# Kernel tuning notes

Measured on AMD Instinct MI355X. Metric: run time of the kernel, lower is better.

Reference implementation:

```python
import jax, jax.numpy as jnp
import numpy as np
from jax import lax

B = 512
THRESHOLD = 0.5
CFG = [64, 64, 'M', 128, 128, 'M', 256, 256, 256, 'M', 512, 512, 512, 'M', 512, 512, 512, 'M']  # VGG16


def _conv_relu(x, w, b):
    # x: [B,C,H,W], w: [O,I,3,3] (torch OIHW layout), pad=1 stride=1
    y = lax.conv_general_dilated(x, w, (1, 1), 'SAME',
                                 dimension_numbers=('NCHW', 'OIHW', 'NCHW'))
    return jax.nn.relu(y + b[None, :, None, None])


def _maxpool2(x):
    return lax.reduce_window(x, -jnp.inf, lax.max, (1, 1, 2, 2), (1, 1, 2, 2), 'VALID')


def _features(x, ws, bs):
    i = 0
    for c in CFG:
        if c == 'M':
            x = _maxpool2(x)
        else:
            x = _conv_relu(x, ws[i], bs[i])
            i += 1
    return x  # [B,512,1,1]


def _gcn(distance):
    # Faithful translation, including the source bug: 'onetensor' is zeros_like,
    # so mask==0 everywhere and A_hat collapses to the identity.
    n = distance.shape[0]
    zero = jnp.zeros_like(distance)
    one = jnp.zeros_like(distance)  # bug in original: torch.zeros_like for onetensor
    adj = jnp.where(distance > THRESHOLD, distance, zero)
    mask = jnp.where(distance > THRESHOLD, one, zero)
    idx = lax.top_k(adj, 10)[1]                                   # [n,10]
    top10 = jnp.zeros_like(adj).at[jnp.arange(n)[:, None], idx].set(1.0)
    top10 = top10 * mask
    a_hat = top10 + jnp.eye(n, dtype=distance.dtype)
    d_inv = jnp.diag(1.0 / jnp.sum(a_hat, axis=1))
    return lax.stop_gradient(a_hat @ d_inv)                        # [n,n]


def _forward(x, target, conv_ws, conv_bs, lin1_w, lin1_b, lin2_w, lin2_b, cls_w, cls_b):
    feat = _features(x, conv_ws, conv_bs).reshape(x.shape[0], -1)  # [B,512]
    h = jax.nn.relu(feat @ lin1_w + lin1_b)                        # [B,256]
    low = h @ lin2_w + lin2_b                                      # [B,128]
    graph_pre = jax.nn.sigmoid(low @ low.T)                        # [B,B]
    graph_gt = (target[:, None] == target[None, :]).astype(jnp.float32)
    mat = _gcn(graph_pre)                                          # [B,B], detached
    out = (mat @ feat) @ cls_w + cls_b                             # [B,10]
    return out, graph_pre, graph_gt


def setup_inputs() -> dict:
    key = jax.random.key(0)
    ks = iter(jax.random.split(key, 64))
    inp = {}
    inp['x'] = jax.random.normal(next(ks), (B, 3, 32, 32), dtype=jnp.float32)
    inp['target'] = jax.random.randint(next(ks), (B,), 0, 10)
    in_c, i = 3, 0
    for c in CFG:
        if c == 'M':
            continue
        scale = 1.0 / np.sqrt(in_c * 9.0)
        inp['conv%d_w' % i] = jax.random.normal(next(ks), (c, in_c, 3, 3), dtype=jnp.float32) * scale
        inp['conv%d_b' % i] = jnp.zeros((c,), dtype=jnp.float32)
        in_c, i = c, i + 1
    inp['lin1_w'] = jax.random.normal(next(ks), (512, 256), dtype=jnp.float32) * (1.0 / np.sqrt(512.0))
    inp['lin1_b'] = jnp.zeros((256,), dtype=jnp.float32)
    inp['lin2_w'] = jax.random.normal(next(ks), (256, 128), dtype=jnp.float32) * (1.0 / np.sqrt(256.0))
    inp['lin2_b'] = jnp.zeros((128,), dtype=jnp.float32)
    inp['cls_w'] = jax.random.normal(next(ks), (512, 10), dtype=jnp.float32) * (1.0 / np.sqrt(512.0))
    inp['cls_b'] = jnp.zeros((10,), dtype=jnp.float32)
    return inp


def reference(x, target,
              conv0_w, conv0_b, conv1_w, conv1_b, conv2_w, conv2_b, conv3_w, conv3_b,
              conv4_w, conv4_b, conv5_w, conv5_b, conv6_w, conv6_b, conv7_w, conv7_b,
              conv8_w, conv8_b, conv9_w, conv9_b, conv10_w, conv10_b, conv11_w, conv11_b,
              conv12_w, conv12_b,
              lin1_w, lin1_b, lin2_w, lin2_b, cls_w, cls_b):
    ws = [conv0_w, conv1_w, conv2_w, conv3_w, conv4_w, conv5_w, conv6_w,
          conv7_w, conv8_w, conv9_w, conv10_w, conv11_w, conv12_w]
    bs = [conv0_b, conv1_b, conv2_b, conv3_b, conv4_b, conv5_b, conv6_b,
          conv7_b, conv8_b, conv9_b, conv10_b, conv11_b, conv12_b]
    return _forward(x, target, ws, bs, lin1_w, lin1_b, lin2_w, lin2_b, cls_w, cls_b)
```

## Files before the change

kernel.cpp:

```cpp
#include <hip/hip_runtime.h>

typedef unsigned short u16;
typedef __bf16 bf16x8 __attribute__((ext_vector_type(8)));
typedef float floatx4 __attribute__((ext_vector_type(4)));

__device__ inline u16 f2bf(float f) {
    return __builtin_bit_cast(u16, (__bf16)f);
}
__device__ inline float bf2f(u16 h) {
    return __uint_as_float(((unsigned int)h) << 16);
}

__device__ __forceinline__ void async_copy16(u16* lds, const u16* g) {
    __builtin_amdgcn_global_load_lds(
        (const __attribute__((address_space(1))) unsigned int*)(uintptr_t)g,
        (__attribute__((address_space(3))) unsigned int*)(unsigned int)(uintptr_t)lds,
        16, 0, 0);
}

__global__ void zero_halo(u16* __restrict__ buf, int Hp, int C, int total8)
{
    int i = blockIdx.x * 256 + threadIdx.x;
    if (i >= total8) return;
    int c8 = i % (C / 8);
    int p  = i / (C / 8);
    int ring = 4 * Hp - 4;
    int h = p % ring;
    int b = p / ring;
    int y, x;
    if (h < Hp)              { y = 0;              x = h; }
    else if (h < 2 * Hp)     { y = Hp - 1;         x = h - Hp; }
    else if (h < 3 * Hp - 2) { y = h - 2 * Hp + 1; x = 0; }
    else                     { y = h - 3 * Hp + 3; x = Hp - 1; }
    uint4 z = make_uint4(0u, 0u, 0u, 0u);
    *(uint4*)(buf + ((size_t)((b * Hp + y) * Hp + x) * C) + c8 * 8) = z;
}

__global__ __launch_bounds__(256) void conv0_mfma(
    const float* __restrict__ x, const float* __restrict__ w,
    const float* __restrict__ bias, u16* __restrict__ out)
{
    __shared__ __align__(16) float xsf[3 * 10 * 36];
    __shared__ int tab[32];
    const int t  = threadIdx.x;
    const int b  = blockIdx.x >> 2;
    const int y0 = (blockIdx.x & 3) * 8;

    for (int i = t; i < 3 * 10 * 36; i += 256) {
        int ci  = i / 360;
        int rem = i % 360;
        int r   = rem / 36;
        int c   = rem % 36;
        int gy  = y0 - 1 + r;
        int gx  = c - 1;
        float v = 0.f;
        if ((unsigned)gy < 32u && (unsigned)gx < 32u)
            v = x[((b * 3 + ci) * 32 + gy) * 32 + gx];
        xsf[i] = v;
    }
    if (t < 32) {
        int k = t, off = 0;
        if (k < 27) {
            int ci = k / 9;
            int r9 = k - ci * 9;
            int rr = r9 / 3;
            int cc = r9 - rr * 3;
            off = (ci * 10 + rr) * 36 + cc;
        }
        tab[t] = off;
    }

    const int lane = t & 63;
    const int wv   = t >> 6;
    const int quad = lane >> 4;
    const int l16  = lane & 15;
    const int q8   = quad * 8;

    bf16x8 bf[4];
    #pragma unroll
    for (int nt = 0; nt < 4; nt++) {
        int col = nt * 16 + l16;
        u16 hh[8];
        #pragma unroll
        for (int j = 0; j < 8; j++) {
            int k = q8 + j;
            float wv_ = (k < 27) ? w[col * 27 + k] : 0.f;
            hh[j] = f2bf(wv_);
        }
        #pragma unroll
        for (int j = 0; j < 8; j++) ((u16*)&bf[nt])[j] = hh[j];
    }
    float bzv[4];
    #pragma unroll
    for (int nt = 0; nt < 4; nt++) bzv[nt] = bias[nt * 16 + l16];

    __syncthreads();

    int tb_[8];
    #pragma unroll
    for (int j = 0; j < 8; j++) tb_[j] = tab[q8 + j];

    bf16x8 af[4];
    #pragma unroll
    for (int mt = 0; mt < 4; mt++) {
        int dm   = wv * 64 + mt * 16 + l16;
        int yloc = dm >> 5;
        int xx   = dm & 31;
        int bix  = yloc * 36 + xx;
        u16 hh[8];
        #pragma unroll
        for (int j = 0; j < 8; j++) hh[j] = f2bf(xsf[bix + tb_[j]]);
        if (quad == 3) {
            #pragma unroll
            for (int j = 3; j < 8; j++) hh[j] = 0;
        }
        #pragma unroll
        for (int j = 0; j < 8; j++) ((u16*)&af[mt])[j] = hh[j];
    }

    floatx4 acc[4][4];
    #pragma unroll
    for (int i = 0; i < 4; i++)
        #pragma unroll
        for (int j = 0; j < 4; j++)
            acc[i][j] = (floatx4){0.f, 0.f, 0.f, 0.f};

    #pragma unroll
    for (int mt = 0; mt < 4; mt++)
        #pragma unroll
        for (int nt = 0; nt < 4; nt++)
            acc[mt][nt] = __builtin_amdgcn_mfma_f32_16x16x32_bf16(
                af[mt], bf[nt], acc[mt][nt], 0, 0, 0);

    #pragma unroll
    for (int mt = 0; mt < 4; mt++) {
        #pragma unroll
        for (int r = 0; r < 4; r++) {
            int p  = wv * 64 + mt * 16 + quad * 4 + r;
            int y  = y0 + (p >> 5);
            int xx = p & 31;
            u16* op = out + (size_t)((b * 34 + y + 1) * 34 + xx + 1) * 64 + l16;
            #pragma unroll
            for (int nt = 0; nt < 4; nt++)
                op[nt * 16] = f2bf(fmaxf(acc[mt][nt][r] + bzv[nt], 0.f));
        }
    }
}

struct RepackArgs {
    const float* src[14];
    u16* dst[14];
    int p1[14];
    int p2[14];
    int startBlk[15];
    int nseg;
};

__global__ __launch_bounds__(256) void repack_all(RepackArgs a)
{
    __shared__ __align__(16) u16 lds[9216];
    int blk = blockIdx.x;
    int s = 0;
    #pragma unroll 1
    while (s + 1 < a.nseg && blk >= a.startBlk[s + 1]) s++;
    const int cb = blk - a.startBlk[s];
    const int t  = threadIdx.x;

    if (a.p2[s] == 0) {
        const int Cin = a.p1[s];
        const int logCin = __builtin_ctz(Cin);
        const float* src = a.src[s] + (size_t)cb * 9216;
        u16* dst = a.dst[s] + (size_t)cb * 9216;
        #pragma unroll
        for (int it = 0; it < 9; it++) {
            int j4 = it * 256 + t;
            float4 v = *(const float4*)(src + j4 * 4);
            ushort4 h;
            h.x = f2bf(v.x); h.y = f2bf(v.y); h.z = f2bf(v.z); h.w = f2bf(v.w);
            *(ushort4*)(lds + j4 * 4) = h;
        }
        __syncthreads();
        #pragma unroll
        for (int it = 0; it < 9; it++) {
            int o4   = (it * 256 + t) * 4;
            int ci   = o4 & (Cin - 1);
            int rest = o4 >> logCin;
            int co   = rest / 9;
            int sh   = rest - co * 9;
            int sb   = (co << logCin) * 9 + ci * 9 + sh;
            ushort4 h;
            h.x = lds[sb]; h.y = lds[sb + 9]; h.z = lds[sb + 18]; h.w = lds[sb + 27];
            *(ushort4*)(dst + o4) = h;
        }
    } else {
        const int K = a.p1[s], N = a.p2[s];
        const int ntx = N >> 6;
        const int k0 = (cb / ntx) * 64, n0 = (cb % ntx) * 64;
        const float* src = a.src[s];
        u16* dst = a.dst[s];
        const int r = t >> 4, c4 = (t & 15) * 4;
        #pragma unroll
        for (int rr = 0; rr < 64; rr += 16) {
            float4 v = *(const float4*)(src + (size_t)(k0 + r + rr) * N + n0 + c4);
            u16* p = lds + (r + rr) * 72 + c4;
            p[0] = f2bf(v.x); p[1] = f2bf(v.y); p[2] = f2bf(v.z); p[3] = f2bf(v.w);
        }
        __syncthreads();
        #pragma unroll
        for (int it = 0; it < 2; it++) {
            int ov = it * 256 + t;
            int n  = ov >> 3;
            int kq = (ov & 7) * 8;
            __align__(16) u16 h[8];
            #pragma unroll
            for (int j = 0; j < 8; j++) h[j] = lds[(kq + j) * 72 + n];
            *(uint4*)(dst + (size_t)(n0 + n) * K + k0 + kq) = *(uint4*)h;
        }
    }
}

struct FragArgs {
    const u16* src[3];
    u16* dst[3];
    int cin[3];
    int logwn[3];
    int total[3];
    int startBlk[4];
};

__global__ __launch_bounds__(256) void repack_frag(FragArgs a)
{
    int blk = blockIdx.x;
    int s = 0;
    #pragma unroll 1
    while (s + 1 < 3 && blk >= a.startBlk[s + 1]) s++;
    int i = (blk - a.startBlk[s]) * 256 + threadIdx.x;
    if (i >= a.total[s]) return;
    const int LOGWN = a.logwn[s];
    int l16  = i & 15;
    int quad = (i >> 4) & 3;
    int nt   = (i >> 6) & 3;
    int wn   = (i >> 8) & ((1 << LOGWN) - 1);
    int kk2  = (i >> (8 + LOGWN)) & 1;
    int it   = i >> (9 + LOGWN);
    int col  = wn * 64 + nt * 16 + l16;
    int k    = it * 64 + (kk2 * 4 + quad) * 8;
    uint4 v = *(const uint4*)(a.src[s] + (size_t)col * 9 * a.cin[s] + k);
    *(uint4*)(a.dst[s] + (size_t)i * 8) = v;
}

template <int BM, int BN>
__global__ __launch_bounds__(256) void conv_gemm(
    const u16* __restrict__ in, const u16* __restrict__ wt,
    const float* __restrict__ bias, u16* __restrict__ out,
    float* __restrict__ partial, size_t pstride,
    int H, int Cin, int Cout, int logHW, int logW, int splitN,
    int outPad, int poolMode)
{
    constexpr int BK = 64;
    constexpr int WC = (BM == 256) ? BN : (BN / 2);
    constexpr int NT = WC / 16;
    constexpr int NB_A = BM / 32;
    constexpr int NB_B = BN / 32;
    constexpr int ASZ = BM * BK;
    constexpr int BSZ = BN * BK;
    __shared__ u16 As[2 * ASZ];
    __shared__ u16 Bs[2 * BSZ];

    const int Nblocks = Cout / BN;
    const int per = gridDim.x >> 3;
    const int bid = (blockIdx.x & 7) * per + (blockIdx.x >> 3);
    const int sp   = bid % splitN;
    const int tile = bid / splitN;
    const int m0 = (tile / Nblocks) * BM;
    const int n0 = (tile % Nblocks) * BN;

    const int t    = threadIdx.x;
    const int lane = t & 63;
    const int wave = t >> 6;
    const int quad = lane >> 4;
    const int l16  = lane & 15;
    const int wm   = (BM == 256) ? wave : (wave >> 1);
    const int wn   = (BM == 256) ? 0 : (wave & 1);
    const int W    = H;
    const int Wp   = H + 2;
    const int HW   = 1 << logHW;
    const int col8 = t & 7;
    const int r0   = t >> 3;
    const int scol = col8 ^ (r0 & 7);

    const int CinB = Cin * 2;

    int vA[NB_A];
    #pragma unroll
    for (int j = 0; j < NB_A; j++) {
        int m  = m0 + r0 + 32 * j;
        int b  = m >> logHW;
        int rm = m & (HW - 1);
        int y  = rm >> logW;
        int xx = rm & (W - 1);
        vA[j] = ((b * Wp + y + 1) * Wp + xx + 1) * CinB + scol * 16;
    }
    int vB[NB_B];
    #pragma unroll
    for (int j = 0; j < NB_B; j++)
        vB[j] = (n0 + r0 + 32 * j) * 9 * CinB + scol * 16;

    const int logKB = (Cin == 64) ? 0 : (Cin == 128) ? 1 : (Cin == 256) ? 2 : 3;
    const int KB  = 1 << logKB;
    const int T   = 9 * KB;
    const int len = T / splitN;
    const int it0 = sp * len;

    int s0 = it0 >> logKB;
    int c3 = s0 - (s0 / 3) * 3;
    int ta = ((s0 / 3 - 1) * Wp + (c3 - 1)) * CinB;
    int kb = (it0 & (KB - 1)) * 128;
    int tb = it0 * 128;

    const char* const inB = (const char*)in;
    const char* const wtB = (const char*)wt;

    floatx4 acc[4][NT];
    #pragma unroll
    for (int i = 0; i < 4; i++)
        #pragma unroll
        for (int j = 0; j < NT; j++)
            acc[i][j] = (floatx4){0.f, 0.f, 0.f, 0.f};

    const int sw = (l16 & 7) * 8;

    auto stage = [&](int ua, int tbv, int buf) {
        u16* la = As + buf * ASZ + t * 8;
        u16* lb = Bs + buf * BSZ + t * 8;
        #pragma unroll
        for (int j = 0; j < NB_A; j++)
            async_copy16(la + j * 2048, (const u16*)(inB + (ua + vA[j])));
        #pragma unroll
        for (int j = 0; j < NB_B; j++)
            async_copy16(lb + j * 2048, (const u16*)(wtB + (tbv + vB[j])));
    };
    auto advance = [&]() {
        tb += 128;
        kb += 128;
        if (kb == CinB) {
            kb = 0;
            ta += (c3 == 2) ? (Wp - 2) * CinB : CinB;
            c3 = (c3 == 2) ? 0 : c3 + 1;
        }
    };

    stage(ta + kb, tb, 0);
    advance();
    __syncthreads();

    int cur = 0;
    for (int it = 0; it < len; it++) {
        if (it + 1 < len) {
            stage(ta + kb, tb, cur ^ 1);
            advance();
        }
        const u16* Ab = As + cur * ASZ;
        const u16* Bb = Bs + cur * BSZ;
        #pragma unroll
        for (int kk = 0; kk < BK; kk += 32) {
            bf16x8 af[4], bfv[NT];
            int cbo = kk + quad * 8;
            #pragma unroll
            for (int mt = 0; mt < 4; mt++)
                af[mt] = *(const bf16x8*)(Ab + (wm * 64 + mt * 16 + l16) * 64 + (cbo ^ sw));
            #pragma unroll
            for (int nt = 0; nt < NT; nt++)
                bfv[nt] = *(const bf16x8*)(Bb + (wn * WC + nt * 16 + l16) * 64 + (cbo ^ sw));
            #pragma unroll
            for (int mt = 0; mt < 4; mt++)
                #pragma unroll
                for (int nt = 0; nt < NT; nt++)
                    acc[mt][nt] = __builtin_amdgcn_mfma_f32_16x16x32_bf16(
                        af[mt], bfv[nt], acc[mt][nt], 0, 0, 0);
        }
        __syncthreads();
        cur ^= 1;
    }

    const int ngb = n0 + wn * WC + l16;

    if (splitN > 1) {
        float* pout = partial + (size_t)sp * pstride;
        #pragma unroll
        for (int mt = 0; mt < 4; mt++)
            #pragma unroll
            for (int r = 0; r < 4; r++) {
                int mg = m0 + wm * 64 + mt * 16 + quad * 4 + r;
                float* op = pout + (size_t)mg * Cout + ngb;
                #pragma unroll
                for (int nt = 0; nt < NT; nt++)
                    op[nt * 16] = acc[mt][nt][r];
            }
        return;
    }

    float bzv[NT];
    #pragma unroll
    for (int nt = 0; nt < NT; nt++) bzv[nt] = bias[ngb + nt * 16];

    if (poolMode) {
        const int Hpo = (H >> 1) + 2;
        if (logW == 5) {
            #pragma unroll
            for (int mt = 0; mt < 2; mt++)
                #pragma unroll
                for (int rp = 0; rp < 2; rp++) {
                    int m1 = m0 + wm * 64 + mt * 16 + quad * 4 + 2 * rp;
                    int b  = m1 >> logHW;
                    int rm = m1 & (HW - 1);
                    int yp = (rm >> logW) >> 1;
                    int xp = (rm & (W - 1)) >> 1;
                    u16* op = out + (size_t)((b * Hpo + yp + 1) * Hpo + xp + 1) * Cout + ngb;
                    #pragma unroll
                    for (int nt = 0; nt < NT; nt++) {
                        float v = fmaxf(
                            fmaxf(acc[mt][nt][2 * rp], acc[mt][nt][2 * rp + 1]),
                            fmaxf(acc[mt + 2][nt][2 * rp], acc[mt + 2][nt][2 * rp + 1]));
                        op[nt * 16] = f2bf(fmaxf(v + bzv[nt], 0.f));
                    }
                }
        } else if (logW == 4) {
            #pragma unroll
            for (int mtp = 0; mtp < 2; mtp++)
                #pragma unroll
                for (int rp = 0; rp < 2; rp++) {
                    int mt = 2 * mtp;
                    int m1 = m0 + wm * 64 + mt * 16 + quad * 4 + 2 * rp;
                    int b  = m1 >> logHW;
                    int rm = m1 & (HW - 1);
                    int yp = (rm >> logW) >> 1;
                    int xp = (rm & (W - 1)) >> 1;
                    u16* op = out + (size_t)((b * Hpo + yp + 1) * Hpo + xp + 1) * Cout + ngb;
                    #pragma unroll
                    for (int nt = 0; nt < NT; nt++) {
                        float v = fmaxf(
                            fmaxf(acc[mt][nt][2 * rp], acc[mt][nt][2 * rp + 1]),
                            fmaxf(acc[mt + 1][nt][2 * rp], acc[mt + 1][nt][2 * rp + 1]));
                        op[nt * 16] = f2bf(fmaxf(v + bzv[nt], 0.f));
                    }
                }
        } else {
            #pragma unroll
            for (int mt = 0; mt < 4; mt++)
                #pragma unroll
                for (int rp = 0; rp < 2; rp++) {
                    int m1 = m0 + wm * 64 + mt * 16 + quad * 4 + 2 * rp;
                    int b  = m1 >> logHW;
                    int rm = m1 & (HW - 1);
                    int yp = (rm >> logW) >> 1;
                    int xp = (rm & (W - 1)) >> 1;
                    u16* op = out + (size_t)((b * Hpo + yp + 1) * Hpo + xp + 1) * Cout + ngb;
                    #pragma unroll
                    for (int nt = 0; nt < NT; nt++) {
                        float a = fmaxf(acc[mt][nt][2 * rp], acc[mt][nt][2 * rp + 1]);
                        float p = __shfl_xor(a, 32, 64);
                        float v = fmaxf(a, p);
                        if (quad < 2)
                            op[nt * 16] = f2bf(fmaxf(v + bzv[nt], 0.f));
                    }
                }
        }
        return;
    }

    #pragma unroll
    for (int mt = 0; mt < 4; mt++) {
        #pragma unroll
        for (int r = 0; r < 4; r++) {
            int mg = m0 + wm * 64 + mt * 16 + quad * 4 + r;
            size_t obase;
            if (outPad) {
                int b  = mg >> logHW;
                int rm = mg & (HW - 1);
                int y  = rm >> logW;
                int xx = rm & (W - 1);
                obase = (size_t)((b * Wp + y + 1) * Wp + xx + 1) * Cout;
            } else {
                obase = (size_t)mg * Cout;
            }
            u16* op = out + obase + ngb;
            #pragma unroll
            for (int nt = 0; nt < NT; nt++)
                op[nt * 16] = f2bf(fmaxf(acc[mt][nt][r] + bzv[nt], 0.f));
        }
    }
}

template <int BM, int BN, int W, int CIN>
__global__ __launch_bounds__(256) void conv_halo(
    const u16* __restrict__ in, const u16* __restrict__ wtf,
    const float* __restrict__ bias, u16* __restrict__ out,
    int outPad, int poolMode)
{
    constexpr int WC = (BM == 256) ? BN : (BN / 2);
    constexpr int NT = WC / 16;
    constexpr int LOGWN = (BM == 256) ? 0 : 1;
    constexpr int Wp = W + 2;
    constexpr int R  = BM / W;
    constexpr int P  = (R + 2) * Wp;
    constexpr int CinB = CIN * 2;
    constexpr int CH = CinB / 16;
    constexpr int LOG_CH = (CH == 8) ? 3 : 4;
    constexpr int HALO_CHUNKS = P * CH;
    constexpr int ROUNDS = (HALO_CHUNKS + 255) / 256;
    constexpr int logW = (W == 32) ? 5 : 4;
    constexpr int logHW = 2 * logW;
    constexpr int HW = 1 << logHW;
    constexpr int KB = CIN / 64;
    constexpr int T  = 9 * KB;

    __shared__ __align__(16) u16 Ah[P * CH * 8];

    const int per = gridDim.x >> 3;
    const int bid = (blockIdx.x & 7) * per + (blockIdx.x >> 3);
    const int m0 = bid * BM;
    const int n0 = 0;

    const int t    = threadIdx.x;
    const int lane = t & 63;
    const int wave = t >> 6;
    const int quad = lane >> 4;
    const int l16  = lane & 15;
    const int wm   = (BM == 256) ? wave : (wave >> 1);
    const int wn   = (BM == 256) ? 0 : (wave & 1);

    const int b  = m0 >> logHW;
    const int y0 = (m0 & (HW - 1)) >> logW;

    const char* hsrc = (const char*)in + (size_t)((b * Wp + y0) * Wp) * CinB;
    #pragma unroll
    for (int rd = 0; rd < ROUNDS; rd++) {
        int i = rd * 256 + t;
        if ((HALO_CHUNKS % 256 == 0) || i < HALO_CHUNKS) {
            int pp   = i >> LOG_CH;
            int si   = i ^ (pp & 7);
            async_copy16(Ah + i * 8, (const u16*)(hsrc + (size_t)si * 16));
        }
    }

    int vBf[2][NT];
    #pragma unroll
    for (int kk2 = 0; kk2 < 2; kk2++)
        #pragma unroll
        for (int nt = 0; nt < NT; nt++)
            vBf[kk2][nt] = ((((kk2 << LOGWN) + wn) * 256 + nt * 64
                            + quad * 16 + l16) << 4);
    const char* const wtB = (const char*)wtf;

    int pBase[4];
    #pragma unroll
    for (int mt = 0; mt < 4; mt++) {
        int dm = wm * 64 + mt * 16 + l16;
        pBase[mt] = (dm >> logW) * Wp + (dm & (W - 1));
    }

    floatx4 acc[4][NT];
    #pragma unroll
    for (int i = 0; i < 4; i++)
        #pragma unroll
        for (int j = 0; j < NT; j++)
            acc[i][j] = (floatx4){0.f, 0.f, 0.f, 0.f};

    const char* const AhB = (const char*)Ah;

    __syncthreads();

    int tb = 0;
    int pOff = 0, c3 = 0, cb = 0;
    for (int it = 0; it < T; it++) {
        const int pO = pOff, cbv = cb;
        cb += 128;
        if (cb == CinB) {
            cb = 0;
            pOff += (c3 == 2) ? (Wp - 2) : 1;
            c3 = (c3 == 2) ? 0 : c3 + 1;
        }

        const char* gb = wtB + tb;
        bf16x8 bfv[2][NT];
        #pragma unroll
        for (int kk2 = 0; kk2 < 2; kk2++)
            #pragma unroll
            for (int nt = 0; nt < NT; nt++)
                bfv[kk2][nt] = *(const bf16x8*)(gb + vBf[kk2][nt]);

        bf16x8 af[2][4];
        #pragma unroll
        for (int mt = 0; mt < 4; mt++) {
            int p  = pBase[mt] + pO;
            int pc = p & 7;
            int ab = p * CinB + cbv;
            #pragma unroll
            for (int kk2 = 0; kk2 < 2; kk2++) {
                int kq = kk2 * 4 + quad;
                af[kk2][mt] = *(const bf16x8*)(AhB + ab + ((kq ^ pc) << 4));
            }
        }

        #pragma unroll
        for (int kk2 = 0; kk2 < 2; kk2++)
            #pragma unroll
            for (int mt = 0; mt < 4; mt++)
                #pragma unroll
                for (int nt = 0; nt < NT; nt++)
                    acc[mt][nt] = __builtin_amdgcn_mfma_f32_16x16x32_bf16(
                        af[kk2][mt], bfv[kk2][nt], acc[mt][nt], 0, 0, 0);

        tb += BN * 128;
    }

    const int ngb = n0 + wn * WC + l16;
    float bzv[NT];
    #pragma unroll
    for (int nt = 0; nt < NT; nt++) bzv[nt] = bias[ngb + nt * 16];
    const int Cout = BN;
    const int H = W;

    if (poolMode) {
        const int Hpo = (H >> 1) + 2;
        if (logW == 5) {
            #pragma unroll
            for (int mt = 0; mt < 2; mt++)
                #pragma unroll
                for (int rp = 0; rp < 2; rp++) {
                    int m1 = m0 + wm * 64 + mt * 16 + quad * 4 + 2 * rp;
                    int bb = m1 >> logHW;
                    int rm = m1 & (HW - 1);
                    int yp = (rm >> logW) >> 1;
                    int xp = (rm & (W - 1)) >> 1;
                    u16* op = out + (size_t)((bb * Hpo + yp + 1) * Hpo + xp + 1) * Cout + ngb;
                    #pragma unroll
                    for (int nt = 0; nt < NT; nt++) {
                        float v = fmaxf(
                            fmaxf(acc[mt][nt][2 * rp], acc[mt][nt][2 * rp + 1]),
                            fmaxf(acc[mt + 2][nt][2 * rp], acc[mt + 2][nt][2 * rp + 1]));
                        op[nt * 16] = f2bf(fmaxf(v + bzv[nt], 0.f));
                    }
                }
        } else {
            #pragma unroll
            for (int mtp = 0; mtp < 2; mtp++)
                #pragma unroll
                for (int rp = 0; rp < 2; rp++) {
                    int mt = 2 * mtp;
                    int m1 = m0 + wm * 64 + mt * 16 + quad * 4 + 2 * rp;
                    int bb = m1 >> logHW;
                    int rm = m1 & (HW - 1);
                    int yp = (rm >> logW) >> 1;
                    int xp = (rm & (W - 1)) >> 1;
                    u16* op = out + (size_t)((bb * Hpo + yp + 1) * Hpo + xp + 1) * Cout + ngb;
                    #pragma unroll
                    for (int nt = 0; nt < NT; nt++) {
                        float v = fmaxf(
                            fmaxf(acc[mt][nt][2 * rp], acc[mt][nt][2 * rp + 1]),
                            fmaxf(acc[mt + 1][nt][2 * rp], acc[mt + 1][nt][2 * rp + 1]));
                        op[nt * 16] = f2bf(fmaxf(v + bzv[nt], 0.f));
                    }
                }
        }
        return;
    }

    #pragma unroll
    for (int mt = 0; mt < 4; mt++) {
        #pragma unroll
        for (int r = 0; r < 4; r++) {
            int mg = m0 + wm * 64 + mt * 16 + quad * 4 + r;
            size_t obase;
            if (outPad) {
                int bb = mg >> logHW;
                int rm = mg & (HW - 1);
                int y  = rm >> logW;
                int xx = rm & (W - 1);
                obase = (size_t)((bb * Wp + y + 1) * Wp + xx + 1) * Cout;
            } else {
                obase = (size_t)mg * Cout;
            }
            u16* op = out + obase + ngb;
            #pragma unroll
            for (int nt = 0; nt < NT; nt++)
                op[nt * 16] = f2bf(fmaxf(acc[mt][nt][r] + bzv[nt], 0.f));
        }
    }
}

__global__ void reduce_split(const float* __restrict__ partial,
                             const float* __restrict__ bias, u16* __restrict__ out,
                             int MN, int C, int logC, int splitN, size_t pstride,
                             int H, int logHW, int logW, int outPad)
{
    int i4 = (blockIdx.x * 256 + threadIdx.x) * 4;
    if (i4 >= MN) return;
    float4 s = *(const float4*)(partial + i4);
    for (int sp = 1; sp < splitN; sp++) {
        float4 p = *(const float4*)(partial + (size_t)sp * pstride + i4);
        s.x += p.x; s.y += p.y; s.z += p.z; s.w += p.w;
    }
    int n = i4 & (C - 1);
    int m = i4 >> logC;
    size_t obase;
    if (outPad) {
        int Wp = H + 2;
        int b  = m >> logHW;
        int rm = m & ((1 << logHW) - 1);
        int y  = rm >> logW;
        int xx = rm & (H - 1);
        obase = (size_t)((b * Wp + y + 1) * Wp + xx + 1) * C;
    } else {
        obase = (size_t)m * C;
    }
    ushort4 o;
    o.x = f2bf(fmaxf(s.x + bias[n + 0], 0.f));
    o.y = f2bf(fmaxf(s.y + bias[n + 1], 0.f));
    o.z = f2bf(fmaxf(s.z + bias[n + 2], 0.f));
    o.w = f2bf(fmaxf(s.w + bias[n + 3], 0.f));
    *(ushort4*)(out + obase + n) = o;
}

__global__ void reduce_pool(const float* __restrict__ partial,
                            const float* __restrict__ bias, u16* __restrict__ out,
                            int total4, int C, int splitN, size_t pstride,
                            int H, int outPad)
{
    int idx = blockIdx.x * 256 + threadIdx.x;
    if (idx >= total4) return;
    int c4 = idx % (C / 4);
    int p  = idx / (C / 4);
    int Ho = H >> 1;
    int xp = p % Ho; p /= Ho;
    int yp = p % Ho;
    int b  = p / Ho;
    int n  = c4 * 4;
    float4 best;
    bool first = true;
    #pragma unroll
    for (int dy = 0; dy < 2; dy++)
        #pragma unroll
        for (int dx = 0; dx < 2; dx++) {
            int m = (b * H + 2 * yp + dy) * H + 2 * xp + dx;
            const float* q = partial + (size_t)m * C + n;
            float4 s = *(const float4*)q;
            for (int sp = 1; sp < splitN; sp++) {
                float4 pp = *(const float4*)(q + (size_t)sp * pstride);
                s.x += pp.x; s.y += pp.y; s.z += pp.z; s.w += pp.w;
            }
            if (first) { best = s; first = false; }
            else {
                best.x = fmaxf(best.x, s.x); best.y = fmaxf(best.y, s.y);
                best.z = fmaxf(best.z, s.z); best.w = fmaxf(best.w, s.w);
            }
        }
    size_t obase;
    if (outPad) {
        int Hpo = Ho + 2;
        obase = (size_t)((b * Hpo + yp + 1) * Hpo + xp + 1) * C;
    } else {
        obase = (size_t)((b * Ho + yp) * Ho + xp) * C;
    }
    ushort4 o;
    o.x = f2bf(fmaxf(best.x + bias[n + 0], 0.f));
    o.y = f2bf(fmaxf(best.y + bias[n + 1], 0.f));
    o.z = f2bf(fmaxf(best.z + bias[n + 2], 0.f));
    o.w = f2bf(fmaxf(best.w + bias[n + 3], 0.f));
    *(ushort4*)(out + obase + n) = o;
}

template <bool RELU, bool OUTBF>
__global__ __launch_bounds__(256) void gemm64(
    const u16* __restrict__ A, const u16* __restrict__ Bt,
    const float* __restrict__ bias, void* __restrict__ outv,
    int M, int N, int K)
{
    constexpr int LDP = 72;
    __shared__ u16 As[64 * LDP];
    __shared__ u16 Bs[64 * LDP];

    const int nb = N >> 6;
    const int m0 = (blockIdx.x / nb) * 64;
    const int n0 = (blockIdx.x % nb) * 64;
    const int t = threadIdx.x, lane = t & 63, wave = t >> 6;
    const int quad = lane >> 4, l16 = lane & 15;
    const int wm = wave >> 1, wn = wave & 1;
    const int col8 = t & 7, r0 = t >> 3;

    floatx4 acc[2][2];
    #pragma unroll
    for (int i = 0; i < 2; i++)
        #pragma unroll
        for (int j = 0; j < 2; j++)
            acc[i][j] = (floatx4){0.f, 0.f, 0.f, 0.f};

    for (int kb = 0; kb < K; kb += 64) {
        #pragma unroll
        for (int j = 0; j < 2; j++) {
            int row = r0 + 32 * j;
            *(uint4*)(As + row * LDP + col8 * 8) =
                *(const uint4*)(A + (size_t)(m0 + row) * K + kb + col8 * 8);
            *(uint4*)(Bs + row * LDP + col8 * 8) =
                *(const uint4*)(Bt + (size_t)(n0 + row) * K + kb + col8 * 8);
        }
        __syncthreads();
        #pragma unroll
        for (int kk = 0; kk < 64; kk += 32) {
            bf16x8 af[2], bfv[2];
            #pragma unroll
            for (int mt = 0; mt < 2; mt++)
                af[mt] = *(const bf16x8*)(As + (wm * 32 + mt * 16 + l16) * LDP + kk + quad * 8);
            #pragma unroll
            for (int nt = 0; nt < 2; nt++)
                bfv[nt] = *(const bf16x8*)(Bs + (wn * 32 + nt * 16 + l16) * LDP + kk + quad * 8);
            #pragma unroll
            for (int mt = 0; mt < 2; mt++)
                #pragma unroll
                for (int nt = 0; nt < 2; nt++)
                    acc[mt][nt] = __builtin_amdgcn_mfma_f32_16x16x32_bf16(
                        af[mt], bfv[nt], acc[mt][nt], 0, 0, 0);
        }
        __syncthreads();
    }
    #pragma unroll
    for (int mt = 0; mt < 2; mt++) {
        #pragma unroll
        for (int nt = 0; nt < 2; nt++) {
            #pragma unroll
            for (int r = 0; r < 4; r++) {
                int mg = m0 + wm * 32 + mt * 16 + quad * 4 + r;
                int ng = n0 + wn * 32 + nt * 16 + l16;
                float v = acc[mt][nt][r] + bias[ng];
                if (RELU) v = fmaxf(v, 0.f);
                if (OUTBF) ((u16*)outv)[(size_t)mg * N + ng] = f2bf(v);
                else       ((float*)outv)[(size_t)mg * N + ng] = v;
            }
        }
    }
}

__global__ __launch_bounds__(256) void graph_tile(
    const float* __restrict__ low, const int* __restrict__ target,
    float* __restrict__ gpre, float* __restrict__ ggt)
{
    __shared__ float Al[64 * 132];
    __shared__ float Bl[128 * 68];
    const int t = threadIdx.x;
    const int gr0 = (blockIdx.x >> 3) * 64;
    const int gc0 = (blockIdx.x & 7) * 64;

    #pragma unroll
    for (int j = 0; j < 32; j++) {
        int flat = t + 256 * j;
        int k = flat & 127;
        int rc = flat >> 7;
        Al[rc * 132 + k] = low[(size_t)(gr0 + rc) * 128 + k];
        Bl[k * 68 + rc]  = low[(size_t)(gc0 + rc) * 128 + k];
    }
    __syncthreads();

    const int tx = t & 15, ty = t >> 4;
    float acc[4][4];
    #pragma unroll
    for (int r = 0; r < 4; r++)
        #pragma unroll
        for (int c = 0; c < 4; c++) acc[r][c] = 0.f;

    for (int k = 0; k < 128; k++) {
        float a[4], b[4];
        #pragma unroll
        for (int r = 0; r < 4; r++) a[r] = Al[(ty * 4 + r) * 132 + k];
        #pragma unroll
        for (int c = 0; c < 4; c++) b[c] = Bl[k * 68 + tx * 4 + c];
        #pragma unroll
        for (int r = 0; r < 4; r++)
            #pragma unroll
            for (int c = 0; c < 4; c++) acc[r][c] += a[r] * b[c];
    }
    #pragma unroll
    for (int r = 0; r < 4; r++) {
        int row = gr0 + ty * 4 + r;
        int tr  = target[row];
        float4 gp, gg;
        float* pp = (float*)&gp;
        float* gg_ = (float*)&gg;
        #pragma unroll
        for (int c = 0; c < 4; c++) {
            pp[c]  = 1.f / (1.f + __expf(-acc[r][c]));
            gg_[c] = (tr == target[gc0 + tx * 4 + c]) ? 1.f : 0.f;
        }
        *(float4*)(gpre + (size_t)row * 512 + gc0 + tx * 4) = gp;
        *(float4*)(ggt  + (size_t)row * 512 + gc0 + tx * 4) = gg;
    }
}

__global__ __launch_bounds__(256) void cls_kernel(
    const u16* __restrict__ feat, const float* __restrict__ w,
    const float* __restrict__ bias, float* __restrict__ out)
{
    __shared__ float ws[5120];
    const int t = threadIdx.x;
    for (int i = t; i < 5120; i += 256) ws[i] = w[i];
    __syncthreads();
    const int lane = t & 63;
    const int row  = blockIdx.x * 4 + (t >> 6);
    float a[10];
    #pragma unroll
    for (int j = 0; j < 10; j++) a[j] = 0.f;
    #pragma unroll
    for (int i = 0; i < 8; i++) {
        int k = i * 64 + lane;
        float f = bf2f(feat[(size_t)row * 512 + k]);
        #pragma unroll
        for (int j = 0; j < 10; j++) a[j] += f * ws[k * 10 + j];
    }
    #pragma unroll
    for (int j = 0; j < 10; j++)
        #pragma unroll
        for (int off = 32; off > 0; off >>= 1)
            a[j] += __shfl_down(a[j], off, 64);
    if (lane == 0) {
        #pragma unroll
        for (int j = 0; j < 10; j++) out[row * 10 + j] = a[j] + bias[j];
    }
}

extern "C" void kernel_launch(void* const* d_in, const int* in_sizes, int n_in,
                              void* d_out, int out_size, void* d_ws, size_t ws_size,
                              hipStream_t stream)
{
    const float* x      = (const float*)d_in[0];
    const int*   target = (const int*)d_in[1];
    const float* conv_w[13];
    const float* conv_b[13];
    for (int i = 0; i < 13; i++) {
        conv_w[i] = (const float*)d_in[2 + 2 * i];
        conv_b[i] = (const float*)d_in[3 + 2 * i];
    }
    const float* lin1_w = (const float*)d_in[28];
    const float* lin1_b = (const float*)d_in[29];
    const float* lin2_w = (const float*)d_in[30];
    const float* lin2_b = (const float*)d_in[31];
    const float* cls_w  = (const float*)d_in[32];
    const float* cls_b  = (const float*)d_in[33];
    float* out = (float*)d_out;

    static const int cin_arr[13]  = {3, 64, 64, 128, 128, 256, 256, 256, 512, 512, 512, 512, 512};
    static const int cout_arr[13] = {64, 64, 128, 128, 256, 256, 256, 512, 512, 512, 512, 512, 512};

    char* ws = (char*)d_ws;
    size_t off = 0;
    const size_t R0SZ = (size_t)512 * 34 * 34 * 64 * 2;
    const size_t R1SZ = (size_t)512 * 34 * 34 * 64 * 2;
    char* R0raw = ws + off; off += R0SZ;
    char* R1raw = ws + off; off += R1SZ;
    u16* R0 = (u16*)R0raw;
    u16* R1 = (u16*)R1raw;
    float* PA = (float*)(R0raw + 20971520);
    float* PB = (float*)(R1raw + 20971520);
    u16* wt[13];
    for (int i = 1; i < 13; i++) {
        wt[i] = (u16*)(ws + off);
        off += (size_t)cout_arr[i] * 9 * cin_arr[i] * 2;
    }
    u16* wtl1 = (u16*)(ws + off); off += (size_t)256 * 512 * 2;
    u16* wtl2 = (u16*)(ws + off); off += (size_t)128 * 256 * 2;
    u16* hbuf = (u16*)(ws + off); off += (size_t)512 * 256 * 2;
    float* lowbuf = (float*)(ws + off); off += (size_t)512 * 128 * 4;
    u16* wtf1 = (u16*)(ws + off); off += (size_t)64 * 9 * 64 * 2;
    u16* wtf2 = (u16*)(ws + off); off += (size_t)128 * 9 * 64 * 2;
    u16* wtf3 = (u16*)(ws + off); off += (size_t)128 * 9 * 128 * 2;

    RepackArgs ra;
    int nb = 0, blk = 0;
    ra.startBlk[0] = 0;
    for (int i = 1; i < 13; i++) {
        ra.src[nb] = conv_w[i];
        ra.dst[nb] = wt[i];
        ra.p1[nb] = cin_arr[i];
        ra.p2[nb] = 0;
        blk += cout_arr[i] * cin_arr[i] / 1024;
        nb++; ra.startBlk[nb] = blk;
    }
    ra.src[nb] = lin1_w; ra.dst[nb] = wtl1; ra.p1[nb] = 512; ra.p2[nb] = 256;
    blk += (512 / 64) * (256 / 64);
    nb++; ra.startBlk[nb] = blk;
    ra.src[nb] = lin2_w; ra.dst[nb] = wtl2; ra.p1[nb] = 256; ra.p2[nb] = 128;
    blk += (256 / 64) * (128 / 64);
    nb++; ra.startBlk[nb] = blk;
    ra.nseg = nb;
    repack_all<<<blk, 256, 0, stream>>>(ra);

    FragArgs fa;
    fa.src[0] = wt[1]; fa.dst[0] = wtf1; fa.cin[0] = 64;  fa.logwn[0] = 0;
    fa.total[0] = 64 * 9 * 64 / 8;
    fa.src[1] = wt[2]; fa.dst[1] = wtf2; fa.cin[1] = 64;  fa.logwn[1] = 1;
    fa.total[1] = 128 * 9 * 64 / 8;
    fa.src[2] = wt[3]; fa.dst[2] = wtf3; fa.cin[2] = 128; fa.logwn[2] = 1;
    fa.total[2] = 128 * 9 * 128 / 8;
    fa.startBlk[0] = 0;
    fa.startBlk[1] = (fa.total[0] + 255) / 256;
    fa.startBlk[2] = fa.startBlk[1] + (fa.total[1] + 255) / 256;
    fa.startBlk[3] = fa.startBlk[2] + (fa.total[2] + 255) / 256;
    repack_frag<<<fa.startBlk[3], 256, 0, stream>>>(fa);

    auto zh = [&](u16* buf, int Hp, int C) {
        int total8 = 512 * (4 * Hp - 4) * (C / 8);
        zero_halo<<<(total8 + 255) / 256, 256, 0, stream>>>(buf, Hp, C, total8);
    };
    auto launch_conv = [&](int li, int Hl, int bm, int bn, u16* inb, u16* outb,
                           float* part, int splitN, int outPad, int poolMode) {
        int Cin = cin_arr[li], Cout = cout_arr[li];
        int M = 512 * Hl * Hl;
        int logW = __builtin_ctz(Hl);
        int logHW = 2 * logW;
        size_t pstride = (size_t)M * Cout;
        int grid = (M / bm) * (Cout / bn) * splitN;
        if (bm == 256) {
            conv_gemm<256, 64><<<grid, 256, 0, stream>>>(
                inb, wt[li], conv_b[li], outb, part, pstride,
                Hl, Cin, Cout, logHW, logW, splitN, outPad, poolMode);
        } else if (bn == 128) {
            conv_gemm<128, 128><<<grid, 256, 0, stream>>>(
                inb, wt[li], conv_b[li], outb, part, pstride,
                Hl, Cin, Cout, logHW, logW, splitN, outPad, poolMode);
        } else {
            conv_gemm<128, 64><<<grid, 256, 0, stream>>>(
                inb, wt[li], conv_b[li], outb, part, pstride,
                Hl, Cin, Cout, logHW, logW, splitN, outPad, poolMode);
        }
    };
    auto launch_reduce = [&](int li, int Hl, u16* outb, float* part, int splitN, int outPad) {
        int Cout = cout_arr[li];
        int M = 512 * Hl * Hl;
        int logW = __builtin_ctz(Hl);
        size_t pstride = (size_t)M * Cout;
        int MN = M * Cout;
        reduce_split<<<(MN / 4 + 255) / 256, 256, 0, stream>>>(
            part, conv_b[li], outb, MN, Cout, __builtin_ctz(Cout),
            splitN, pstride, Hl, 2 * logW, logW, outPad);
    };
    auto launch_reduce_pool = [&](int li, int Hl, u16* outb, float* part, int splitN, int outPad) {
        int Cout = cout_arr[li];
        int M = 512 * Hl * Hl;
        size_t pstride = (size_t)M * Cout;
        int total4 = 512 * (Hl / 2) * (Hl / 2) * Cout / 4;
        reduce_pool<<<(total4 + 255) / 256, 256, 0, stream>>>(
            part, conv_b[li], outb, total4, Cout, splitN, pstride, Hl, outPad);
    };

    zh(R0, 34, 64);
    conv0_mfma<<<512 * 4, 256, 0, stream>>>(x, conv_w[0], conv_b[0], R0);

    zh(R1, 18, 64);
    conv_halo<256, 64, 32, 64><<<2048, 256, 0, stream>>>(
        R0, wtf1, conv_b[1], R1, 0, 1);
    zh(R0, 18, 128);
    conv_halo<128, 128, 16, 64><<<1024, 256, 0, stream>>>(
        R1, wtf2, conv_b[2], R0, 1, 0);
    zh(R1, 10, 128);
    conv_halo<128, 128, 16, 128><<<1024, 256, 0, stream>>>(
        R0, wtf3, conv_b[3], R1, 0, 1);
    zh(R0, 10, 256);
    launch_conv(4, 8, 128, 128, R1, R0, nullptr, 1, 1, 0);
    zh(R1, 10, 256);
    launch_conv(5, 8, 128, 128, R0, R1, nullptr, 1, 1, 0);
    zh(R0, 6, 256);
    launch_conv(6, 8, 128, 128, R1, R0, nullptr, 1, 0, 1);
    zh(R1, 6, 512);
    launch_conv(7, 4, 128, 128, R0, R1, PB, 2, 1, 0);
    launch_reduce(7, 4, R1, PB, 2, 1);
    zh(R0, 6, 512);
    launch_conv(8, 4, 128, 128, R1, R0, PA, 2, 1, 0);
    launch_reduce(8, 4, R0, PA, 2, 1);
    zh(R1, 4, 512);
    launch_conv(9, 4, 128, 128, R0, R1, PB, 2, 0, 0);
    launch_reduce_pool(9, 4, R1, PB, 2, 1);
    zh(R0, 4, 512);
    launch_conv(10, 2, 128, 64, R1, R0, PA, 4, 1, 0);
    launch_reduce(10, 2, R0, PA, 4, 1);
    zh(R1, 4, 512);
    launch_conv(11, 2, 128, 64, R0, R1, PB, 4, 1, 0);
    launch_reduce(11, 2, R1, PB, 4, 1);
    launch_conv(12, 2, 128, 64, R1, R0, PA, 4, 0, 0);
    launch_reduce_pool(12, 2, R0, PA, 4, 0);

    u16* feat = R0;
    gemm64<true, true><<<(512 / 64) * (256 / 64), 256, 0, stream>>>(
        feat, wtl1, lin1_b, hbuf, 512, 256, 512);
    gemm64<false, false><<<(512 / 64) * (128 / 64), 256, 0, stream>>>(
        hbuf, wtl2, lin2_b, lowbuf, 512, 128, 256);
    graph_tile<<<64, 256, 0, stream>>>(lowbuf, target, out + 5120, out + 5120 + 262144);
    cls_kernel<<<128, 256, 0, stream>>>(feat, cls_w, cls_b, out);
}
```

Measured before the change: 681.1 us.

## Load conv weights directly into registers from fragment-packed layout for layers 4-9

Extends the fragment repack kernel to pre-arrange the weights of conv layers 4-9 in MFMA fragment order. The 128x128 conv GEMM can now load B operands straight from global memory into registers instead of staging them through LDS. This removes the B-side LDS traffic and shrinks shared memory, which could raise occupancy. The cost is global loads that are no longer async or prefetched, so latency may be exposed, and the packed weights are stored in a hardcoded offset region of R1's workspace.

```diff
diff --git a/kernel.cpp b/kernel.cpp
--- a/kernel.cpp
+++ b/kernel.cpp
@@ -220,12 +220,13 @@
 }
 
 struct FragArgs {
-    const u16* src[3];
-    u16* dst[3];
-    int cin[3];
-    int logwn[3];
-    int total[3];
-    int startBlk[4];
+    const u16* src[9];
+    u16* dst[9];
+    int cin[9];
+    int lognt[9];
+    int logwn[9];
+    int T[9];
+    int startBlk[10];
 };
 
 __global__ __launch_bounds__(256) void repack_frag(FragArgs a)
@@ -233,23 +234,27 @@
     int blk = blockIdx.x;
     int s = 0;
     #pragma unroll 1
-    while (s + 1 < 3 && blk >= a.startBlk[s + 1]) s++;
+    while (s + 1 < 9 && blk >= a.startBlk[s + 1]) s++;
     int i = (blk - a.startBlk[s]) * 256 + threadIdx.x;
-    if (i >= a.total[s]) return;
-    const int LOGWN = a.logwn[s];
+    const int lognt = a.lognt[s], logwn = a.logwn[s];
+    const int T = a.T[s], Cin = a.cin[s];
     int l16  = i & 15;
     int quad = (i >> 4) & 3;
-    int nt   = (i >> 6) & 3;
-    int wn   = (i >> 8) & ((1 << LOGWN) - 1);
-    int kk2  = (i >> (8 + LOGWN)) & 1;
-    int it   = i >> (9 + LOGWN);
-    int col  = wn * 64 + nt * 16 + l16;
+    int nt   = (i >> 6) & ((1 << lognt) - 1);
+    int wn   = (i >> (6 + lognt)) & ((1 << logwn) - 1);
+    int kk2  = (i >> (6 + lognt + logwn)) & 1;
+    int rest = i >> (7 + lognt + logwn);
+    int it   = rest % T;
+    int nblk = rest / T;
+    int WC_  = 16 << lognt;
+    int BN_  = WC_ << logwn;
+    int col  = nblk * BN_ + wn * WC_ + nt * 16 + l16;
     int k    = it * 64 + (kk2 * 4 + quad) * 8;
-    uint4 v = *(const uint4*)(a.src[s] + (size_t)col * 9 * a.cin[s] + k);
+    uint4 v = *(const uint4*)(a.src[s] + (size_t)col * 9 * Cin + k);
     *(uint4*)(a.dst[s] + (size_t)i * 8) = v;
 }
 
-template <int BM, int BN>
+template <int BM, int BN, bool DB>
 __global__ __launch_bounds__(256) void conv_gemm(
     const u16* __restrict__ in, const u16* __restrict__ wt,
     const float* __restrict__ bias, u16* __restrict__ out,
@@ -260,12 +265,13 @@
     constexpr int BK = 64;
     constexpr int WC = (BM == 256) ? BN : (BN / 2);
     constexpr int NT = WC / 16;
+    constexpr int LOGWN = (BM == 256) ? 0 : 1;
     constexpr int NB_A = BM / 32;
     constexpr int NB_B = BN / 32;
     constexpr int ASZ = BM * BK;
     constexpr int BSZ = BN * BK;
     __shared__ u16 As[2 * ASZ];
-    __shared__ u16 Bs[2 * BSZ];
+    __shared__ u16 Bs[DB ? 16 : 2 * BSZ];
 
     const int Nblocks = Cout / BN;
     const int per = gridDim.x >> 3;
@@ -330,15 +336,29 @@
 
     const int sw = (l16 & 7) * 8;
 
+    int vBf[2][NT];
+    size_t tbD = 0;
+    if constexpr (DB) {
+        #pragma unroll
+        for (int kk2 = 0; kk2 < 2; kk2++)
+            #pragma unroll
+            for (int nt = 0; nt < NT; nt++)
+                vBf[kk2][nt] = (((((kk2 << LOGWN) + wn) * NT + nt) * 4 + quad)
+                                * 16 + l16) << 4;
+        tbD = ((size_t)(n0 / BN) * T + it0) * (size_t)BN * 128;
+    }
+
     auto stage = [&](int ua, int tbv, int buf) {
         u16* la = As + buf * ASZ + t * 8;
-        u16* lb = Bs + buf * BSZ + t * 8;
         #pragma unroll
         for (int j = 0; j < NB_A; j++)
             async_copy16(la + j * 2048, (const u16*)(inB + (ua + vA[j])));
-        #pragma unroll
-        for (int j = 0; j < NB_B; j++)
-            async_copy16(lb + j * 2048, (const u16*)(wtB + (tbv + vB[j])));
+        if constexpr (!DB) {
+            u16* lb = Bs + buf * BSZ + t * 8;
+            #pragma unroll
+            for (int j = 0; j < NB_B; j++)
+                async_copy16(lb + j * 2048, (const u16*)(wtB + (tbv + vB[j])));
+        }
     };
     auto advance = [&]() {
         tb += 128;
@@ -356,6 +376,16 @@
 
     int cur = 0;
     for (int it = 0; it < len; it++) {
+        bf16x8 bfv[2][NT];
+        if constexpr (DB) {
+            const char* gb = wtB + tbD;
+            #pragma unroll
+            for (int kk2 = 0; kk2 < 2; kk2++)
+                #pragma unroll
+                for (int nt = 0; nt < NT; nt++)
+                    bfv[kk2][nt] = *(const bf16x8*)(gb + vBf[kk2][nt]);
+            tbD += (size_t)BN * 128;
+        }
         if (it + 1 < len) {
             stage(ta + kb, tb, cur ^ 1);
             advance();
@@ -363,21 +393,23 @@
         const u16* Ab = As + cur * ASZ;
         const u16* Bb = Bs + cur * BSZ;
         #pragma unroll
-        for (int kk = 0; kk < BK; kk += 32) {
-            bf16x8 af[4], bfv[NT];
-            int cbo = kk + quad * 8;
+        for (int kk2 = 0; kk2 < 2; kk2++) {
+            bf16x8 af[4];
+            int cbo = kk2 * 32 + quad * 8;
             #pragma unroll
             for (int mt = 0; mt < 4; mt++)
                 af[mt] = *(const bf16x8*)(Ab + (wm * 64 + mt * 16 + l16) * 64 + (cbo ^ sw));
-            #pragma unroll
-            for (int nt = 0; nt < NT; nt++)
-                bfv[nt] = *(const bf16x8*)(Bb + (wn * WC + nt * 16 + l16) * 64 + (cbo ^ sw));
+            if constexpr (!DB) {
+                #pragma unroll
+                for (int nt = 0; nt < NT; nt++)
+                    bfv[kk2][nt] = *(const bf16x8*)(Bb + (wn * WC + nt * 16 + l16) * 64 + (cbo ^ sw));
+            }
             #pragma unroll
             for (int mt = 0; mt < 4; mt++)
                 #pragma unroll
                 for (int nt = 0; nt < NT; nt++)
                     acc[mt][nt] = __builtin_amdgcn_mfma_f32_16x16x32_bf16(
-                        af[mt], bfv[nt], acc[mt][nt], 0, 0, 0);
+                        af[mt], bfv[kk2][nt], acc[mt][nt], 0, 0, 0);
         }
         __syncthreads();
         cur ^= 1;
@@ -972,6 +1004,13 @@
     u16* wtf1 = (u16*)(ws + off); off += (size_t)64 * 9 * 64 * 2;
     u16* wtf2 = (u16*)(ws + off); off += (size_t)128 * 9 * 64 * 2;
     u16* wtf3 = (u16*)(ws + off); off += (size_t)128 * 9 * 128 * 2;
+    char* wtfD = R1raw + 54525952;
+    u16* wtf4 = (u16*)(wtfD + 0);
+    u16* wtf5 = (u16*)(wtfD + 589824);
+    u16* wtf6 = (u16*)(wtfD + 1769472);
+    u16* wtf7 = (u16*)(wtfD + 2949120);
+    u16* wtf8 = (u16*)(wtfD + 5308416);
+    u16* wtf9 = (u16*)(wtfD + 10027008);
 
     RepackArgs ra;
     int nb = 0, blk = 0;
@@ -994,43 +1033,47 @@
     repack_all<<<blk, 256, 0, stream>>>(ra);
 
     FragArgs fa;
-    fa.src[0] = wt[1]; fa.dst[0] = wtf1; fa.cin[0] = 64;  fa.logwn[0] = 0;
-    fa.total[0] = 64 * 9 * 64 / 8;
-    fa.src[1] = wt[2]; fa.dst[1] = wtf2; fa.cin[1] = 64;  fa.logwn[1] = 1;
-    fa.total[1] = 128 * 9 * 64 / 8;
-    fa.src[2] = wt[3]; fa.dst[2] = wtf3; fa.cin[2] = 128; fa.logwn[2] = 1;
-    fa.total[2] = 128 * 9 * 128 / 8;
-    fa.startBlk[0] = 0;
-    fa.startBlk[1] = (fa.total[0] + 255) / 256;
-    fa.startBlk[2] = fa.startBlk[1] + (fa.total[1] + 255) / 256;
-    fa.startBlk[3] = fa.startBlk[2] + (fa.total[2] + 255) / 256;
-    repack_frag<<<fa.startBlk[3], 256, 0, stream>>>(fa);
+    {
+        const u16* fs[9] = {wt[1], wt[2], wt[3], wt[4], wt[5], wt[6], wt[7], wt[8], wt[9]};
+        u16* fd[9] = {wtf1, wtf2, wtf3, wtf4, wtf5, wtf6, wtf7, wtf8, wtf9};
+        int fc[9]  = {64, 64, 128, 128, 256, 256, 256, 512, 512};
+        int fw[9]  = {0, 1, 1, 1, 1, 1, 1, 1, 1};
+        int fT[9]  = {9, 9, 18, 18, 36, 36, 36, 72, 72};
+        int fch[9] = {4608, 9216, 18432, 36864, 73728, 73728, 147456, 294912, 294912};
+        int cum = 0;
+        for (int i = 0; i < 9; i++) {
+            fa.src[i] = fs[i]; fa.dst[i] = fd[i];
+            fa.cin[i] = fc[i]; fa.lognt[i] = 2; fa.logwn[i] = fw[i]; fa.T[i] = fT[i];
+            fa.startBlk[i] = cum;
+            cum += fch[i] / 256;
+        }
+        fa.startBlk[9] = cum;
+        repack_frag<<<cum, 256, 0, stream>>>(fa);
+    }
 
     auto zh = [&](u16* buf, int Hp, int C) {
         int total8 = 512 * (4 * Hp - 4) * (C / 8);
         zero_halo<<<(total8 + 255) / 256, 256, 0, stream>>>(buf, Hp, C, total8);
     };
-    auto launch_conv = [&](int li, int Hl, int bm, int bn, u16* inb, u16* outb,
-                           float* part, int splitN, int outPad, int poolMode) {
+    auto launch_convDB = [&](int li, int Hl, u16* inb, const u16* wfrag, u16* outb,
+                             float* part, int splitN, int outPad, int poolMode) {
         int Cin = cin_arr[li], Cout = cout_arr[li];
         int M = 512 * Hl * Hl;
         int logW = __builtin_ctz(Hl);
-        int logHW = 2 * logW;
-        size_t pstride = (size_t)M * Cout;
-        int grid = (M / bm) * (Cout / bn) * splitN;
-        if (bm == 256) {
-            conv_gemm<256, 64><<<grid, 256, 0, stream>>>(
-                inb, wt[li], conv_b[li], outb, part, pstride,
-                Hl, Cin, Cout, logHW, logW, splitN, outPad, poolMode);
-        } else if (bn == 128) {
-            conv_gemm<128, 128><<<grid, 256, 0, stream>>>(
-                inb, wt[li], conv_b[li], outb, part, pstride,
-                Hl, Cin, Cout, logHW, logW, splitN, outPad, poolMode);
-        } else {
-            conv_gemm<128, 64><<<grid, 256, 0, stream>>>(
-                inb, wt[li], conv_b[li], outb, part, pstride,
-                Hl, Cin, Cout, logHW, logW, splitN, outPad, poolMode);
-        }
+        int grid = (M / 128) * (Cout / 128) * splitN;
+        conv_gemm<128, 128, true><<<grid, 256, 0, stream>>>(
+            inb, wfrag, conv_b[li], outb, part, (size_t)M * Cout,
+            Hl, Cin, Cout, 2 * logW, logW, splitN, outPad, poolMode);
+    };
+    auto launch_conv64 = [&](int li, int Hl, u16* inb, u16* outb,
+                             float* part, int splitN, int outPad, int poolMode) {
+        int Cin = cin_arr[li], Cout = cout_arr[li];
+        int M = 512 * Hl * Hl;
+        int logW = __builtin_ctz(Hl);
+        int grid = (M / 128) * (Cout / 64) * splitN;
+        conv_gemm<128, 64, false><<<grid, 256, 0, stream>>>(
+            inb, wt[li], conv_b[li], outb, part, (size_t)M * Cout,
+            Hl, Cin, Cout, 2 * logW, logW, splitN, outPad, poolMode);
     };
     auto launch_reduce = [&](int li, int Hl, u16* outb, float* part, int splitN, int outPad) {
         int Cout = cout_arr[li];
@@ -1064,27 +1107,27 @@
     conv_halo<128, 128, 16, 128><<<1024, 256, 0, stream>>>(
         R0, wtf3, conv_b[3], R1, 0, 1);
     zh(R0, 10, 256);
-    launch_conv(4, 8, 128, 128, R1, R0, nullptr, 1, 1, 0);
+    launch_convDB(4, 8, R1, wtf4, R0, nullptr, 1, 1, 0);
     zh(R1, 10, 256);
-    launch_conv(5, 8, 128, 128, R0, R1, nullptr, 1, 1, 0);
+    launch_convDB(5, 8, R0, wtf5, R1, nullptr, 1, 1, 0);
     zh(R0, 6, 256);
-    launch_conv(6, 8, 128, 128, R1, R0, nullptr, 1, 0, 1);
+    launch_convDB(6, 8, R1, wtf6, R0, nullptr, 1, 0, 1);
     zh(R1, 6, 512);
-    launch_conv(7, 4, 128, 128, R0, R1, PB, 2, 1, 0);
+    launch_convDB(7, 4, R0, wtf7, R1, PB, 2, 1, 0);
     launch_reduce(7, 4, R1, PB, 2, 1);
     zh(R0, 6, 512);
-    launch_conv(8, 4, 128, 128, R1, R0, PA, 2, 1, 0);
+    launch_convDB(8, 4, R1, wtf8, R0, PA, 2, 1, 0);
     launch_reduce(8, 4, R0, PA, 2, 1);
     zh(R1, 4, 512);
-    launch_conv(9, 4, 128, 128, R0, R1, PB, 2, 0, 0);
+    launch_convDB(9, 4, R0, wtf9, R1, PB, 2, 0, 0);
     launch_reduce_pool(9, 4, R1, PB, 2, 1);
     zh(R0, 4, 512);
-    launch_conv(10, 2, 128, 64, R1, R0, PA, 4, 1, 0);
+    launch_conv64(10, 2, R1, R0, PA, 4, 1, 0);
     launch_reduce(10, 2, R0, PA, 4, 1);
     zh(R1, 4, 512);
-    launch_conv(11, 2, 128, 64, R0, R1, PB, 4, 1, 0);
+    launch_conv64(11, 2, R0, R1, PB, 4, 1, 0);
     launch_reduce(11, 2, R1, PB, 4, 1);
-    launch_conv(12, 2, 128, 64, R1, R0, PA, 4, 0, 0);
+    launch_conv64(12, 2, R1, R0, PA, 4, 0, 0);
     launch_reduce_pool(12, 2, R0, PA, 4, 0);
 
     u16* feat = R0;
```

Result: no change. 689.5 us (+1.2%).
